# Kernel tuning notes

Hardware: AMD Instinct MI355X
Metric: run time of the kernel (lower is better)

The kernel has to match this reference:

```python
import jax, jax.numpy as jnp
import numpy as np

K = 50
EPS = 1e-8


def setup_inputs() -> dict:
    key = jax.random.key(0)
    k1, k2 = jax.random.split(key)
    B, S, V = 2, 2048, 50257
    p = jax.random.uniform(k1, (B, S, V), dtype=jnp.float32)
    q = jax.random.uniform(k2, (B, S, V), dtype=jnp.float32)
    # normalize to probability distributions over the vocab dim
    p = p / jnp.sum(p, axis=-1, keepdims=True)
    q = q / jnp.sum(q, axis=-1, keepdims=True)
    return {"p": p, "q": q}


def _kl(p, q):
    p_safe = p + EPS
    q_safe = q + EPS
    return jnp.sum(p_safe * jnp.log(p_safe / q_safe), axis=-1)


def reference(p, q):
    B, S, V = p.shape
    N = B * S
    p_flat = p.reshape(N, V)
    q_flat = q.reshape(N, V)

    _, p_idx = jax.lax.top_k(p_flat, K)  # [N, K]
    _, q_idx = jax.lax.top_k(q_flat, K)  # [N, K]

    rows = jnp.arange(N)[:, None]  # [N, 1]
    mask = jnp.zeros((N, V), dtype=bool)
    mask = mask.at[rows, p_idx].set(True)
    mask = mask.at[rows, q_idx].set(True)

    p_m = jnp.where(mask, p_flat, 0.0)
    q_m = jnp.where(mask, q_flat, 0.0)

    p_m = p_m / (jnp.sum(p_m, axis=-1, keepdims=True) + EPS)
    q_m = q_m / (jnp.sum(q_m, axis=-1, keepdims=True) + EPS)

    m = 0.5 * (p_m + q_m)
    jsd = 0.5 * _kl(p_m, m) + 0.5 * _kl(q_m, m)  # [N]
    return jsd.reshape(B, S)
```

## Files before the change

### kernel.cpp

```cpp
#include <hip/hip_runtime.h>
#include <stdint.h>

#define NTHREADS 256
#define KTOP 50
#define CAP 1024
#define EPSV 1e-8f

typedef unsigned long long u64;
typedef uint32_t u32;
typedef float __attribute__((ext_vector_type(4))) f4;

#define C_CNTP 0
#define C_CNTQ 1
#define C_OVF  2
#define C_GEN  3

__device__ __forceinline__ float block_max(float v, float* s_f, int tid) {
    for (int off = 32; off; off >>= 1) v = fmaxf(v, __shfl_down(v, off));
    if ((tid & 63) == 0) s_f[tid >> 6] = v;
    __syncthreads();
    if (tid == 0) {
        float m = s_f[0];
        for (int w = 1; w < NTHREADS / 64; ++w) m = fmaxf(m, s_f[w]);
        s_f[4] = m;
    }
    __syncthreads();
    float r = s_f[4];
    __syncthreads();
    return r;
}

__device__ __forceinline__ void push32(u32* cand, u32* cnt, u32* ovf,
                                       float v, int idx, float t, u32 tbits) {
    if (v >= t) {
        u32 delta = __float_as_uint(v) - tbits;
        if (delta > 0xFFFFu) { *ovf = 1u; delta = 0xFFFFu; }
        u32 pos = atomicAdd(cnt, 1u);
        if (pos < CAP) cand[pos] = (delta << 16) | (0xFFFFu - (u32)idx);
    }
}

__device__ __forceinline__ void push64(u64* cand, u32* cnt,
                                       float v, int idx, float t) {
    if (v >= t) {
        u32 pos = atomicAdd(cnt, 1u);
        if (pos < CAP)
            cand[pos] = (((u64)__float_as_uint(v)) << 16) |
                        (u64)(0xFFFFu - (u32)idx);
    }
}

__device__ int collect_direct64(const float* __restrict__ row, int V, float t,
                                u64* cand, u32* s_cnt, int tid) {
    if (tid == 0) *s_cnt = 0;
    __syncthreads();
    int mis = (int)(((uintptr_t)row >> 2) & 3);
    int head = (4 - mis) & 3; if (head > V) head = V;
    if (tid < head) push64(cand, s_cnt, row[tid], tid, t);
    int nvec = (V - head) >> 2;
    const float4* vr = reinterpret_cast<const float4*>(row + head);
    for (int i = tid; i < nvec; i += NTHREADS) {
        float4 v = vr[i];
        int b = head + (i << 2);
        push64(cand, s_cnt, v.x, b, t);     push64(cand, s_cnt, v.y, b + 1, t);
        push64(cand, s_cnt, v.z, b + 2, t); push64(cand, s_cnt, v.w, b + 3, t);
    }
    for (int i = head + (nvec << 2) + tid; i < V; i += NTHREADS)
        push64(cand, s_cnt, row[i], i, t);
    __syncthreads();
    int n = (int)*s_cnt;
    __syncthreads();
    return n;
}

__device__ void find_topk64(const u64* cand, int nc, uint16_t* top,
                            u64* s_merge, int tid) {
    int lane = tid & 63, w = tid >> 6;
    u64 r0 = 0, r1 = 0, r2 = 0, r3 = 0;
    int j0 = (w << 6) + lane;
    if (j0 < nc)       r0 = cand[j0];
    if (j0 + 256 < nc) r1 = cand[j0 + 256];
    if (j0 + 512 < nc) r2 = cand[j0 + 512];
    if (j0 + 768 < nc) r3 = cand[j0 + 768];
    for (int k = 0; k < KTOP; ++k) {
        u64 a = r0 > r1 ? r0 : r1;
        u64 b = r2 > r3 ? r2 : r3;
        u64 m = a > b ? a : b;
        #pragma unroll
        for (int off = 32; off; off >>= 1) {
            u64 o = __shfl_xor(m, off);
            if (o > m) m = o;
        }
        if (lane == 0) s_merge[w * KTOP + k] = m;
        if (r0 == m) r0 = 0; else if (r1 == m) r1 = 0;
        else if (r2 == m) r2 = 0; else if (r3 == m) r3 = 0;
    }
    __syncthreads();
    if (w == 0) {
        u64 q0 = 0, q1 = 0, q2 = 0, q3 = 0;
        if (lane < 4 * KTOP)       q0 = s_merge[lane];
        if (lane + 64 < 4 * KTOP)  q1 = s_merge[lane + 64];
        if (lane + 128 < 4 * KTOP) q2 = s_merge[lane + 128];
        if (lane + 192 < 4 * KTOP) q3 = s_merge[lane + 192];
        for (int k = 0; k < KTOP; ++k) {
            u64 a = q0 > q1 ? q0 : q1;
            u64 b = q2 > q3 ? q2 : q3;
            u64 m = a > b ? a : b;
            #pragma unroll
            for (int off = 32; off; off >>= 1) {
                u64 o = __shfl_xor(m, off);
                if (o > m) m = o;
            }
            if (lane == 0) top[k] = (uint16_t)(0xFFFFu - (u32)(m & 0xFFFFu));
            if (q0 == m) q0 = 0; else if (q1 == m) q1 = 0;
            else if (q2 == m) q2 = 0; else if (q3 == m) q3 = 0;
        }
    }
    __syncthreads();
}

template <int NR>
__device__ void find32(const u32* cand, int nc, uint16_t* top, int lane) {
    u32 r[NR];
    #pragma unroll
    for (int j = 0; j < NR; ++j) {
        int idx = lane + j * 64;
        r[j] = (idx < nc) ? cand[idx] : 0u;
    }
    u32 mine = 0;
    for (int k = 0; k < KTOP; ++k) {
        u32 m = 0;
        #pragma unroll
        for (int j = 0; j < NR; ++j) m = r[j] > m ? r[j] : m;
        #pragma unroll
        for (int off = 32; off; off >>= 1) {
            u32 o = __shfl_xor(m, off);
            m = o > m ? o : m;
        }
        if (lane == k) mine = m;
        #pragma unroll
        for (int j = 0; j < NR; ++j) if (r[j] == m) r[j] = 0;
    }
    if (lane < KTOP) top[lane] = (uint16_t)(0xFFFFu - (mine & 0xFFFFu));
}

#define ISSUE(RP, RQ, IDX) \
    asm volatile("global_load_dwordx4 %0, %2, off\n\t" \
                 "global_load_dwordx4 %1, %3, off" \
                 : "=&v"(RP), "=&v"(RQ) \
                 : "v"(vp4 + (IDX)), "v"(vq4 + (IDX)))

#define WAITV(N) do { \
    asm volatile("s_waitcnt vmcnt(" #N ")" ::: "memory"); \
    __builtin_amdgcn_sched_barrier(0); } while (0)

#define CONSUME(RP, RQ, G) do { \
    float _mp = fmaxf(fmaxf(RP.x, RP.y), fmaxf(RP.z, RP.w)); \
    float _mq = fmaxf(fmaxf(RQ.x, RQ.y), fmaxf(RQ.z, RQ.w)); \
    int _e = head + (((G) * NTHREADS + tid) << 2); \
    if (_mp >= tP) { \
        push32(candP, &s_c[C_CNTP], &s_c[C_OVF], RP.x, _e,     tP, tPb); \
        push32(candP, &s_c[C_CNTP], &s_c[C_OVF], RP.y, _e + 1, tP, tPb); \
        push32(candP, &s_c[C_CNTP], &s_c[C_OVF], RP.z, _e + 2, tP, tPb); \
        push32(candP, &s_c[C_CNTP], &s_c[C_OVF], RP.w, _e + 3, tP, tPb); \
    } \
    if (_mq >= tQ) { \
        push32(candQ, &s_c[C_CNTQ], &s_c[C_OVF], RQ.x, _e,     tQ, tQb); \
        push32(candQ, &s_c[C_CNTQ], &s_c[C_OVF], RQ.y, _e + 1, tQ, tQb); \
        push32(candQ, &s_c[C_CNTQ], &s_c[C_OVF], RQ.z, _e + 2, tQ, tQb); \
        push32(candQ, &s_c[C_CNTQ], &s_c[C_OVF], RQ.w, _e + 3, tQ, tQb); \
    } } while (0)

__global__ __launch_bounds__(NTHREADS, 4)
void topk_jsd_kernel(const float* __restrict__ p, const float* __restrict__ q,
                     float* __restrict__ out, int V)
{
    __shared__ u64 candRaw[CAP];
    __shared__ u64 s_merge[4 * KTOP];
    __shared__ float s_f[8];
    __shared__ u32 s_c[4];
    __shared__ uint16_t topP[KTOP];
    __shared__ uint16_t topQ[KTOP];
    __shared__ uint16_t s_union[2 * KTOP];
    __shared__ int s_nu;

    u32* candP = (u32*)candRaw;
    u32* candQ = ((u32*)candRaw) + CAP;

    const int row = blockIdx.x;
    const int tid = threadIdx.x;
    const int lane = tid & 63, w = tid >> 6;
    const float* prow = p + (size_t)row * (size_t)V;
    const float* qrow = q + (size_t)row * (size_t)V;

    int smp = V < 2048 ? V : 2048;
    float msP = 0.f, msQ = 0.f;
    for (int i = tid; i < smp; i += NTHREADS) {
        msP = fmaxf(msP, prow[i]);
        msQ = fmaxf(msQ, qrow[i]);
    }
    float MsP = block_max(msP, s_f, tid);
    float MsQ = block_max(msQ, s_f, tid);

    float eps0 = fminf(128.f / (float)V + 1.f / (float)smp, 0.5f);
    float tP = MsP * (1.f - eps0);
    float tQ = MsQ * (1.f - eps0);
    u32 tPb = __float_as_uint(tP), tQb = __float_as_uint(tQ);

    int misP = (int)(((uintptr_t)prow >> 2) & 3);
    int misQ = (int)(((uintptr_t)qrow >> 2) & 3);
    int headP = (4 - misP) & 3; if (headP > V) headP = V;
    int headQ = (4 - misQ) & 3; if (headQ > V) headQ = V;
    bool fast = (headP == headQ);

    int ncP = -1, ncQ = -1;
    u32 ovf = 1;

    if (fast) {
        int head = headP;
        if (tid == 0) { s_c[0] = 0; s_c[1] = 0; s_c[2] = 0; }
        __syncthreads();
        int nvec = (V - head) >> 2;
        const f4* vp4 = reinterpret_cast<const f4*>(prow + head);
        const f4* vq4 = reinterpret_cast<const f4*>(qrow + head);

        if (tid < head) {
            push32(candP, &s_c[C_CNTP], &s_c[C_OVF], prow[tid], tid, tP, tPb);
            push32(candQ, &s_c[C_CNTQ], &s_c[C_OVF], qrow[tid], tid, tQ, tQb);
        }

        int n4 = (nvec / NTHREADS) & ~3;
        if (n4 >= 8) {
            f4 p0, p1, p2, p3, q0, q1, q2, q3;
            ISSUE(p0, q0, 0 * NTHREADS + tid);
            ISSUE(p1, q1, 1 * NTHREADS + tid);
            ISSUE(p2, q2, 2 * NTHREADS + tid);
            ISSUE(p3, q3, 3 * NTHREADS + tid);
            int gend = n4 - 4;
            for (int g = 0; g < gend; g += 4) {
                WAITV(6); CONSUME(p0, q0, g + 0); ISSUE(p0, q0, (g + 4) * NTHREADS + tid);
                WAITV(6); CONSUME(p1, q1, g + 1); ISSUE(p1, q1, (g + 5) * NTHREADS + tid);
                WAITV(6); CONSUME(p2, q2, g + 2); ISSUE(p2, q2, (g + 6) * NTHREADS + tid);
                WAITV(6); CONSUME(p3, q3, g + 3); ISSUE(p3, q3, (g + 7) * NTHREADS + tid);
            }
            WAITV(0);
            CONSUME(p0, q0, gend + 0);
            CONSUME(p1, q1, gend + 1);
            CONSUME(p2, q2, gend + 2);
            CONSUME(p3, q3, gend + 3);
        } else {
            n4 = 0;
        }

        for (int i = n4 * NTHREADS + tid; i < nvec; i += NTHREADS) {
            f4 a = vp4[i], b = vq4[i];
            int e = head + (i << 2);
            push32(candP, &s_c[C_CNTP], &s_c[C_OVF], a.x, e,     tP, tPb);
            push32(candP, &s_c[C_CNTP], &s_c[C_OVF], a.y, e + 1, tP, tPb);
            push32(candP, &s_c[C_CNTP], &s_c[C_OVF], a.z, e + 2, tP, tPb);
            push32(candP, &s_c[C_CNTP], &s_c[C_OVF], a.w, e + 3, tP, tPb);
            push32(candQ, &s_c[C_CNTQ], &s_c[C_OVF], b.x, e,     tQ, tQb);
            push32(candQ, &s_c[C_CNTQ], &s_c[C_OVF], b.y, e + 1, tQ, tQb);
            push32(candQ, &s_c[C_CNTQ], &s_c[C_OVF], b.z, e + 2, tQ, tQb);
            push32(candQ, &s_c[C_CNTQ], &s_c[C_OVF], b.w, e + 3, tQ, tQb);
        }
        for (int i = head + (nvec << 2) + tid; i < V; i += NTHREADS) {
            push32(candP, &s_c[C_CNTP], &s_c[C_OVF], prow[i], i, tP, tPb);
            push32(candQ, &s_c[C_CNTQ], &s_c[C_OVF], qrow[i], i, tQ, tQb);
        }
        __syncthreads();
        ncP = (int)s_c[C_CNTP];
        ncQ = (int)s_c[C_CNTQ];
        ovf = s_c[C_OVF];
        __syncthreads();
    }

    bool okP = fast && !ovf && ncP >= KTOP && ncP <= CAP;
    bool okQ = fast && !ovf && ncQ >= KTOP && ncQ <= CAP;

    if (okP && w == 0) {
        if (ncP <= 256) find32<4>(candP, ncP, topP, lane);
        else            find32<16>(candP, ncP, topP, lane);
    }
    if (okQ && w == 1) {
        if (ncQ <= 256) find32<4>(candQ, ncQ, topQ, lane);
        else            find32<16>(candQ, ncQ, topQ, lane);
    }

    if (!okP) {
        float eps = eps0;
        int nc = collect_direct64(prow, V, MsP * (1.f - eps), candRaw, &s_c[C_GEN], tid);
        for (int a = 0; a < 10 && (nc < KTOP || nc > CAP); ++a) {
            eps = (nc > CAP) ? eps * 0.25f : fminf(eps * 4.f, 1.f);
            nc = collect_direct64(prow, V, MsP * (1.f - eps), candRaw, &s_c[C_GEN], tid);
        }
        if (nc > CAP) nc = CAP;
        find_topk64(candRaw, nc, topP, s_merge, tid);
    }
    if (!okQ) {
        float eps = eps0;
        int nc = collect_direct64(qrow, V, MsQ * (1.f - eps), candRaw, &s_c[C_GEN], tid);
        for (int a = 0; a < 10 && (nc < KTOP || nc > CAP); ++a) {
            eps = (nc > CAP) ? eps * 0.25f : fminf(eps * 4.f, 1.f);
            nc = collect_direct64(qrow, V, MsQ * (1.f - eps), candRaw, &s_c[C_GEN], tid);
        }
        if (nc > CAP) nc = CAP;
        find_topk64(candRaw, nc, topQ, s_merge, tid);
    }
    __syncthreads();

    if (tid < KTOP) s_union[tid] = topP[tid];
    __syncthreads();
    if (tid < 64) {
        bool freshb = false; uint16_t qi = 0;
        if (tid < KTOP) {
            qi = topQ[tid]; freshb = true;
            for (int j = 0; j < KTOP; ++j) if (topP[j] == qi) freshb = false;
        }
        u64 mb = __ballot(freshb);
        int pos = __popcll(mb & ((1ull << tid) - 1ull));
        if (freshb) s_union[KTOP + pos] = qi;
        if (tid == 0) s_nu = KTOP + __popcll(mb);
    }
    __syncthreads();
    int nu = s_nu;

    float pv = 0.f, qv = 0.f;
    if (tid < nu) {
        int ui = s_union[tid]; ui = ui < V ? ui : V - 1;
        pv = prow[ui];
        qv = qrow[ui];
    }

    float sp = pv, sq = qv;
    for (int off = 32; off; off >>= 1) { sp += __shfl_down(sp, off); sq += __shfl_down(sq, off); }
    if ((tid & 63) == 0) { s_f[w] = sp; s_f[4 + w] = sq; }
    __syncthreads();
    if (tid == 0) {
        float a = 0.f, b = 0.f;
        for (int ww = 0; ww < NTHREADS / 64; ++ww) { a += s_f[ww]; b += s_f[4 + ww]; }
        s_f[0] = a; s_f[4] = b;
    }
    __syncthreads();
    float sump = s_f[0], sumq = s_f[4];
    __syncthreads();

    float term = 0.f;
    if (tid < nu) {
        float pn = pv / (sump + EPSV);
        float qn = qv / (sumq + EPSV);
        float mn = 0.5f * (pn + qn);
        float ps = pn + EPSV, qs = qn + EPSV, ms = mn + EPSV;
        term = 0.5f * (ps * logf(ps / ms) + qs * logf(qs / ms));
    }
    for (int off = 32; off; off >>= 1) term += __shfl_down(term, off);
    if ((tid & 63) == 0) s_f[w] = term;
    __syncthreads();
    if (tid == 0) {
        float a = 0.f;
        for (int ww = 0; ww < NTHREADS / 64; ++ww) a += s_f[ww];
        out[row] = a;
    }
}

extern "C" void kernel_launch(void* const* d_in, const int* in_sizes, int n_in,
                              void* d_out, int out_size, void* d_ws, size_t ws_size,
                              hipStream_t stream) {
    const float* p = (const float*)d_in[0];
    const float* q = (const float*)d_in[1];
    float* out = (float*)d_out;
    if (out_size <= 0) return;
    int N = out_size;
    int V = in_sizes[0] / N;
    topk_jsd_kernel<<<dim3(N), dim3(NTHREADS), 0, stream>>>(p, q, out, V);
}
```

Before: 399.8 us.

## Stream p and q rows separately with six-deep single-load ring and higher occupancy

Replaces the joint p/q streaming loop, which had four paired loads in flight, with a per-row stream_one helper. Each row is scanned in turn with a six-deep ring of single dwordx4 loads, so each row gets its own alignment handling and the same-misalignment fast-path requirement goes away. Launch bounds are raised from 4 to 8 waves per SIMD so that lower register pressure allows more concurrent blocks to hide memory latency. In exchange, p and q are no longer overlapped within a block, and each thread keeps fewer bytes in flight.

```diff
diff --git a/kernel.cpp b/kernel.cpp
--- a/kernel.cpp
+++ b/kernel.cpp
@@ -144,34 +144,79 @@
     if (lane < KTOP) top[lane] = (uint16_t)(0xFFFFu - (mine & 0xFFFFu));
 }
 
-#define ISSUE(RP, RQ, IDX) \
-    asm volatile("global_load_dwordx4 %0, %2, off\n\t" \
-                 "global_load_dwordx4 %1, %3, off" \
-                 : "=&v"(RP), "=&v"(RQ) \
-                 : "v"(vp4 + (IDX)), "v"(vq4 + (IDX)))
+#define ISSUE1(R, PTR) \
+    asm volatile("global_load_dwordx4 %0, %1, off" \
+                 : "=&v"(R) : "v"(PTR))
 
 #define WAITV(N) do { \
     asm volatile("s_waitcnt vmcnt(" #N ")" ::: "memory"); \
     __builtin_amdgcn_sched_barrier(0); } while (0)
 
-#define CONSUME(RP, RQ, G) do { \
-    float _mp = fmaxf(fmaxf(RP.x, RP.y), fmaxf(RP.z, RP.w)); \
-    float _mq = fmaxf(fmaxf(RQ.x, RQ.y), fmaxf(RQ.z, RQ.w)); \
-    int _e = head + (((G) * NTHREADS + tid) << 2); \
-    if (_mp >= tP) { \
-        push32(candP, &s_c[C_CNTP], &s_c[C_OVF], RP.x, _e,     tP, tPb); \
-        push32(candP, &s_c[C_CNTP], &s_c[C_OVF], RP.y, _e + 1, tP, tPb); \
-        push32(candP, &s_c[C_CNTP], &s_c[C_OVF], RP.z, _e + 2, tP, tPb); \
-        push32(candP, &s_c[C_CNTP], &s_c[C_OVF], RP.w, _e + 3, tP, tPb); \
-    } \
-    if (_mq >= tQ) { \
-        push32(candQ, &s_c[C_CNTQ], &s_c[C_OVF], RQ.x, _e,     tQ, tQb); \
-        push32(candQ, &s_c[C_CNTQ], &s_c[C_OVF], RQ.y, _e + 1, tQ, tQb); \
-        push32(candQ, &s_c[C_CNTQ], &s_c[C_OVF], RQ.z, _e + 2, tQ, tQb); \
-        push32(candQ, &s_c[C_CNTQ], &s_c[C_OVF], RQ.w, _e + 3, tQ, tQb); \
+#define CONSUME1(R, G) do { \
+    float _m = fmaxf(fmaxf(R.x, R.y), fmaxf(R.z, R.w)); \
+    if (_m >= t) { \
+        int _e = head + (((G) * NTHREADS + tid) << 2); \
+        push32(cand, cnt, ovf, R.x, _e,     t, tbits); \
+        push32(cand, cnt, ovf, R.y, _e + 1, t, tbits); \
+        push32(cand, cnt, ovf, R.z, _e + 2, t, tbits); \
+        push32(cand, cnt, ovf, R.w, _e + 3, t, tbits); \
     } } while (0)
 
-__global__ __launch_bounds__(NTHREADS, 4)
+__device__ __forceinline__ void stream_one(
+    const float* __restrict__ row, int V, float t, u32 tbits,
+    u32* cand, u32* cnt, u32* ovf, int tid)
+{
+    int mis = (int)(((uintptr_t)row >> 2) & 3);
+    int head = (4 - mis) & 3; if (head > V) head = V;
+    int nvec = (V - head) >> 2;
+    const f4* v4 = reinterpret_cast<const f4*>(row + head);
+
+    if (tid < head) push32(cand, cnt, ovf, row[tid], tid, t, tbits);
+
+    int ngrp = nvec / NTHREADS;
+    int ring = 0;
+    if (ngrp >= 12) {
+        f4 s0, s1, s2, s3, s4, s5;
+        const f4* pp = v4 + tid;
+        ISSUE1(s0, pp); pp += NTHREADS;
+        ISSUE1(s1, pp); pp += NTHREADS;
+        ISSUE1(s2, pp); pp += NTHREADS;
+        ISSUE1(s3, pp); pp += NTHREADS;
+        ISSUE1(s4, pp); pp += NTHREADS;
+        ISSUE1(s5, pp); pp += NTHREADS;
+        int gend6 = ((ngrp - 6) / 6) * 6;
+        int g = 0;
+        for (; g < gend6; g += 6) {
+            WAITV(5); CONSUME1(s0, g + 0); ISSUE1(s0, pp); pp += NTHREADS;
+            WAITV(5); CONSUME1(s1, g + 1); ISSUE1(s1, pp); pp += NTHREADS;
+            WAITV(5); CONSUME1(s2, g + 2); ISSUE1(s2, pp); pp += NTHREADS;
+            WAITV(5); CONSUME1(s3, g + 3); ISSUE1(s3, pp); pp += NTHREADS;
+            WAITV(5); CONSUME1(s4, g + 4); ISSUE1(s4, pp); pp += NTHREADS;
+            WAITV(5); CONSUME1(s5, g + 5); ISSUE1(s5, pp); pp += NTHREADS;
+        }
+        WAITV(0);
+        CONSUME1(s0, g + 0);
+        CONSUME1(s1, g + 1);
+        CONSUME1(s2, g + 2);
+        CONSUME1(s3, g + 3);
+        CONSUME1(s4, g + 4);
+        CONSUME1(s5, g + 5);
+        ring = g + 6;
+    }
+
+    for (int i = ring * NTHREADS + tid; i < nvec; i += NTHREADS) {
+        f4 a = v4[i];
+        int e = head + (i << 2);
+        push32(cand, cnt, ovf, a.x, e,     t, tbits);
+        push32(cand, cnt, ovf, a.y, e + 1, t, tbits);
+        push32(cand, cnt, ovf, a.z, e + 2, t, tbits);
+        push32(cand, cnt, ovf, a.w, e + 3, t, tbits);
+    }
+    for (int i = head + (nvec << 2) + tid; i < V; i += NTHREADS)
+        push32(cand, cnt, ovf, row[i], i, t, tbits);
+}
+
+__global__ __launch_bounds__(NTHREADS, 8)
 void topk_jsd_kernel(const float* __restrict__ p, const float* __restrict__ q,
                      float* __restrict__ out, int V)
 {
@@ -207,76 +252,20 @@
     float tQ = MsQ * (1.f - eps0);
     u32 tPb = __float_as_uint(tP), tQb = __float_as_uint(tQ);
 
-    int misP = (int)(((uintptr_t)prow >> 2) & 3);
-    int misQ = (int)(((uintptr_t)qrow >> 2) & 3);
-    int headP = (4 - misP) & 3; if (headP > V) headP = V;
-    int headQ = (4 - misQ) & 3; if (headQ > V) headQ = V;
-    bool fast = (headP == headQ);
-
-    int ncP = -1, ncQ = -1;
-    u32 ovf = 1;
-
-    if (fast) {
-        int head = headP;
-        if (tid == 0) { s_c[0] = 0; s_c[1] = 0; s_c[2] = 0; }
-        __syncthreads();
-        int nvec = (V - head) >> 2;
-        const f4* vp4 = reinterpret_cast<const f4*>(prow + head);
-        const f4* vq4 = reinterpret_cast<const f4*>(qrow + head);
-
-        if (tid < head) {
-            push32(candP, &s_c[C_CNTP], &s_c[C_OVF], prow[tid], tid, tP, tPb);
-            push32(candQ, &s_c[C_CNTQ], &s_c[C_OVF], qrow[tid], tid, tQ, tQb);
-        }
-
-        int n4 = (nvec / NTHREADS) & ~3;
-        if (n4 >= 8) {
-            f4 p0, p1, p2, p3, q0, q1, q2, q3;
-            ISSUE(p0, q0, 0 * NTHREADS + tid);
-            ISSUE(p1, q1, 1 * NTHREADS + tid);
-            ISSUE(p2, q2, 2 * NTHREADS + tid);
-            ISSUE(p3, q3, 3 * NTHREADS + tid);
-            int gend = n4 - 4;
-            for (int g = 0; g < gend; g += 4) {
-                WAITV(6); CONSUME(p0, q0, g + 0); ISSUE(p0, q0, (g + 4) * NTHREADS + tid);
-                WAITV(6); CONSUME(p1, q1, g + 1); ISSUE(p1, q1, (g + 5) * NTHREADS + tid);
-                WAITV(6); CONSUME(p2, q2, g + 2); ISSUE(p2, q2, (g + 6) * NTHREADS + tid);
-                WAITV(6); CONSUME(p3, q3, g + 3); ISSUE(p3, q3, (g + 7) * NTHREADS + tid);
-            }
-            WAITV(0);
-            CONSUME(p0, q0, gend + 0);
-            CONSUME(p1, q1, gend + 1);
-            CONSUME(p2, q2, gend + 2);
-            CONSUME(p3, q3, gend + 3);
-        } else {
-            n4 = 0;
-        }
-
-        for (int i = n4 * NTHREADS + tid; i < nvec; i += NTHREADS) {
-            f4 a = vp4[i], b = vq4[i];
-            int e = head + (i << 2);
-            push32(candP, &s_c[C_CNTP], &s_c[C_OVF], a.x, e,     tP, tPb);
-            push32(candP, &s_c[C_CNTP], &s_c[C_OVF], a.y, e + 1, tP, tPb);
-            push32(candP, &s_c[C_CNTP], &s_c[C_OVF], a.z, e + 2, tP, tPb);
-            push32(candP, &s_c[C_CNTP], &s_c[C_OVF], a.w, e + 3, tP, tPb);
-            push32(candQ, &s_c[C_CNTQ], &s_c[C_OVF], b.x, e,     tQ, tQb);
-            push32(candQ, &s_c[C_CNTQ], &s_c[C_OVF], b.y, e + 1, tQ, tQb);
-            push32(candQ, &s_c[C_CNTQ], &s_c[C_OVF], b.z, e + 2, tQ, tQb);
-            push32(candQ, &s_c[C_CNTQ], &s_c[C_OVF], b.w, e + 3, tQ, tQb);
-        }
-        for (int i = head + (nvec << 2) + tid; i < V; i += NTHREADS) {
-            push32(candP, &s_c[C_CNTP], &s_c[C_OVF], prow[i], i, tP, tPb);
-            push32(candQ, &s_c[C_CNTQ], &s_c[C_OVF], qrow[i], i, tQ, tQb);
-        }
-        __syncthreads();
-        ncP = (int)s_c[C_CNTP];
-        ncQ = (int)s_c[C_CNTQ];
-        ovf = s_c[C_OVF];
-        __syncthreads();
-    }
-
-    bool okP = fast && !ovf && ncP >= KTOP && ncP <= CAP;
-    bool okQ = fast && !ovf && ncQ >= KTOP && ncQ <= CAP;
+    if (tid == 0) { s_c[0] = 0; s_c[1] = 0; s_c[2] = 0; }
+    __syncthreads();
+
+    stream_one(prow, V, tP, tPb, candP, &s_c[C_CNTP], &s_c[C_OVF], tid);
+    stream_one(qrow, V, tQ, tQb, candQ, &s_c[C_CNTQ], &s_c[C_OVF], tid);
+
+    __syncthreads();
+    int ncP = (int)s_c[C_CNTP];
+    int ncQ = (int)s_c[C_CNTQ];
+    u32 ovf = s_c[C_OVF];
+    __syncthreads();
+
+    bool okP = !ovf && ncP >= KTOP && ncP <= CAP;
+    bool okQ = !ovf && ncQ >= KTOP && ncQ <= CAP;
 
     if (okP && w == 0) {
         if (ncP <= 256) find32<4>(candP, ncP, topP, lane);
```

New measurement: 408.8 us. +2.2%, slower.
